# Kernel tuning notes

Hardware: AMD Instinct MI355X
Metric: run time of the kernel (lower is better)

Reference implementation:

```python
import jax, jax.numpy as jnp
import numpy as np

N, E, C, L, B = 40000, 640000, 128, 3, 64
EPS = 1e-5


def _layer_norm(h, g, b):
    m = h.mean(-1, keepdims=True)
    v = h.var(-1, keepdims=True)
    return (h - m) / jnp.sqrt(v + EPS) * g + b


def setup_inputs() -> dict:
    key = jax.random.key(0)
    ks = jax.random.split(key, 24)
    s = 0.05
    inp = {
        "x": jax.random.normal(ks[0], (N, C), jnp.float32),
        "edge_index": jax.random.randint(ks[1], (2, E), 0, N, dtype=jnp.int32),
        "batch": jnp.sort(jax.random.randint(ks[2], (N,), 0, B, dtype=jnp.int32)),
        # pre-scaler Linear(in=C -> hidden=C)
        "pre_w": jax.random.normal(ks[3], (C, C), jnp.float32) * s,
        "pre_b": jnp.zeros((C,), jnp.float32),
        # per-layer GCNConv weight/bias
        "conv_w": jax.random.normal(ks[4], (L, C, C), jnp.float32) * s,
        "conv_b": jnp.zeros((L, C), jnp.float32),
        # per-layer post-conv LayerNorm (applied for layers 0..L-2)
        "ln_g": jnp.ones((L, C), jnp.float32),
        "ln_b": jnp.zeros((L, C), jnp.float32),
        # per-layer FFN: lin1, lin2, LayerNorm
        "ffn_w1": jax.random.normal(ks[5], (L, C, C), jnp.float32) * s,
        "ffn_b1": jnp.zeros((L, C), jnp.float32),
        "ffn_w2": jax.random.normal(ks[6], (L, C, C), jnp.float32) * s,
        "ffn_b2": jnp.zeros((L, C), jnp.float32),
        "ffn_ln_g": jnp.ones((L, C), jnp.float32),
        "ffn_ln_b": jnp.zeros((L, C), jnp.float32),
        # classifier MLP: Linear(C,C)+ReLU+Linear(C,1)
        "cls_w1": jax.random.normal(ks[7], (C, C), jnp.float32) * s,
        "cls_b1": jnp.zeros((C,), jnp.float32),
        "cls_w2": jax.random.normal(ks[8], (C, 1), jnp.float32) * s,
        "cls_b2": jnp.zeros((1,), jnp.float32),
    }
    return inp


def reference(x, edge_index, batch, pre_w, pre_b, conv_w, conv_b, ln_g, ln_b,
              ffn_w1, ffn_b1, ffn_w2, ffn_b2, ffn_ln_g, ffn_ln_b,
              cls_w1, cls_b1, cls_w2, cls_b2):
    src, dst = edge_index[0], edge_index[1]
    # GCN symmetric normalization with self-loops: deg counts incoming edges + 1
    deg = jax.ops.segment_sum(jnp.ones((E,), x.dtype), dst, num_segments=N) + 1.0
    inv_sqrt = jax.lax.rsqrt(deg)                      # [N]
    norm_e = inv_sqrt[src] * inv_sqrt[dst]             # [E]
    self_norm = inv_sqrt * inv_sqrt                    # [N], 1/deg for self-loop

    h = x @ pre_w + pre_b                              # pre_scaler

    for i in range(L):
        layer_in = h
        hw = h @ conv_w[i]                             # [N,C]
        msg = hw[src] * norm_e[:, None]                # gather + scale [E,C]
        h = jax.ops.segment_sum(msg, dst, num_segments=N)
        h = h + hw * self_norm[:, None] + conv_b[i]    # self-loop + bias
        if i < L - 1:
            h = _layer_norm(h, ln_g[i], ln_b[i])       # norm
            h = jax.nn.relu(h)                         # act (act_first=False)
            h = h + layer_in                           # residual (dropout=0)
            # FFN: lin2(relu(lin1(h))) + h, then norm
            y = jax.nn.relu(h @ ffn_w1[i] + ffn_b1[i]) @ ffn_w2[i] + ffn_b2[i] + h
            h = _layer_norm(y, ffn_ln_g[i], ffn_ln_b[i])

    # global mean pool per graph
    counts = jax.ops.segment_sum(jnp.ones((N,), h.dtype), batch, num_segments=B)
    g = jax.ops.segment_sum(h, batch, num_segments=B) / jnp.maximum(counts, 1.0)[:, None]

    out = jax.nn.relu(g @ cls_w1 + cls_b1) @ cls_w2 + cls_b2   # [B,1]
    return out
```

## Files before the change

kernel.cpp:

```cpp
#include <hip/hip_runtime.h>
#include <hip/hip_fp16.h>
#include <cstdint>
#include <cstddef>

#define N_NODES 40000
#define N_EDGES 640000
#define CH 128
#define NL 3
#define NB 64
#define LN_EPS 1e-5f

typedef short short8 __attribute__((ext_vector_type(8)));
typedef float floatx4 __attribute__((ext_vector_type(4)));

__device__ __forceinline__ unsigned short bf16_rne(float f) {
    unsigned int u = __float_as_uint(f);
    unsigned int r = u + 0x7FFF + ((u >> 16) & 1);
    return (unsigned short)(r >> 16);
}


__global__ void deg_kernel(const int* __restrict__ ei, int* __restrict__ degi) {
    int e = blockIdx.x * 256 + threadIdx.x;
    if (e < N_EDGES) atomicAdd(&degi[ei[N_EDGES + e]], 1);
}

__global__ void isq_kernel(const int* __restrict__ degi, float* __restrict__ isq) {
    int n = blockIdx.x * 256 + threadIdx.x;
    if (n < N_NODES) isq[n] = rsqrtf((float)degi[n] + 1.0f);
}

__global__ void scan1_kernel(const int* __restrict__ degi, int* __restrict__ rowptr,
                             int* __restrict__ bsum) {
    __shared__ int s[256];
    int t = threadIdx.x;
    int i = blockIdx.x * 256 + t;
    int v = (i < N_NODES) ? degi[i] : 0;
    s[t] = v;
    __syncthreads();
    for (int off = 1; off < 256; off <<= 1) {
        int add = (t >= off) ? s[t - off] : 0;
        __syncthreads();
        s[t] += add;
        __syncthreads();
    }
    if (i < N_NODES) rowptr[i + 1] = s[t];
    if (t == 255) bsum[blockIdx.x] = s[255];
}

__global__ void scan2_kernel(int* __restrict__ bsum, int* __restrict__ boff, int nb) {
    __shared__ int s[256];
    int t = threadIdx.x;
    int v = (t < nb) ? bsum[t] : 0;
    s[t] = v;
    __syncthreads();
    for (int off = 1; off < 256; off <<= 1) {
        int add = (t >= off) ? s[t - off] : 0;
        __syncthreads();
        s[t] += add;
        __syncthreads();
    }
    if (t < nb) boff[t] = s[t] - v;
}

__global__ void scan3_kernel(int* __restrict__ rowptr, const int* __restrict__ boff) {
    int i = blockIdx.x * 256 + threadIdx.x;
    if (i < N_NODES) rowptr[i + 1] += boff[blockIdx.x];
    if (i == 0 && blockIdx.x == 0) rowptr[0] = 0;
}

__global__ void fill_csr_kernel(const int* __restrict__ ei, const int* __restrict__ rowptr,
                                int* __restrict__ fill, int* __restrict__ srcs) {
    int e = blockIdx.x * 256 + threadIdx.x;
    if (e < N_EDGES) {
        int s = ei[e];
        int d = ei[N_EDGES + e];
        int pos = atomicAdd(&fill[d], 1);
        srcs[rowptr[d] + pos] = s;
    }
}

__global__ void pack_w_kernel(const float* __restrict__ pre_w, const float* __restrict__ conv_w,
                              const float* __restrict__ ffn_w1, const float* __restrict__ ffn_w2,
                              short* __restrict__ wpk, float* __restrict__ zbias) {
    int idx = blockIdx.x * 256 + threadIdx.x;
    if (idx < CH) zbias[idx] = 0.f;
    int mat = idx >> 14;
    int e = idx & 16383;
    int k = e >> 7, n = e & 127;
    const float* src;
    switch (mat) {
        case 0: src = pre_w; break;
        case 1: case 2: case 3: src = conv_w + (size_t)(mat - 1) * 16384; break;
        case 4: case 5: src = ffn_w1 + (size_t)(mat - 4) * 16384; break;
        default: src = ffn_w2 + (size_t)(mat - 6) * 16384; break;
    }
    float f = src[e];
    unsigned short h = bf16_rne(f);
    float hf = __uint_as_float((unsigned)h << 16);
    unsigned short l = bf16_rne(f - hf);
    int kk = k >> 5, quad = (k >> 3) & 3, j = k & 7;
    int frag = ((kk * 4 + quad) * 128 + n) * 8 + j;
    wpk[(size_t)mat * 32768 + frag] = (short)h;
    wpk[(size_t)mat * 32768 + 16384 + frag] = (short)l;
}

__device__ __forceinline__ void gld_lds16(const short* g, short* l) {
    __builtin_amdgcn_global_load_lds(
        (const __attribute__((address_space(1))) unsigned int*)g,
        (__attribute__((address_space(3))) unsigned int*)l, 16, 0, 0);
}

template <int MODE, int OUTHALF>
__launch_bounds__(256, 3)
__global__ void gemm_mfma(const float* __restrict__ A, const short* __restrict__ Wpk,
                          const float* __restrict__ bias, const float* __restrict__ Res,
                          void* __restrict__ OutP) {
    __shared__ short smem[16384];
    const int tid = threadIdx.x;
    const int lane = tid & 63;
    const int wv = tid >> 6;
    const int row0 = blockIdx.x * 64 + wv * 16;
    const int m = lane & 15;
    const int quad = lane >> 4;

    floatx4 acc[8];
#pragma unroll
    for (int c = 0; c < 8; ++c) acc[c] = (floatx4){0.f, 0.f, 0.f, 0.f};

    const float* arow = A + (size_t)(row0 + m) * CH + quad * 8;

#pragma unroll 1
    for (int h = 0; h < 2; ++h) {
#pragma unroll
        for (int r = 0; r < 4; ++r) {
            int off = r * 2048 + tid * 8;
            gld_lds16(Wpk + h * 8192 + off, smem + off);
        }
#pragma unroll
        for (int r = 0; r < 4; ++r) {
            int off = r * 2048 + tid * 8;
            gld_lds16(Wpk + 16384 + h * 8192 + off, smem + 8192 + off);
        }
        __syncthreads();

#pragma unroll 1
        for (int kx = 0; kx < 2; ++kx) {
            const int kk = h * 2 + kx;
            float4 a0 = *(const float4*)(arow + kk * 32);
            float4 a1 = *(const float4*)(arow + kk * 32 + 4);
            float av[8] = {a0.x, a0.y, a0.z, a0.w, a1.x, a1.y, a1.z, a1.w};
            short8 ahi, alo;
#pragma unroll
            for (int j = 0; j < 8; ++j) {
                unsigned short hb = bf16_rne(av[j]);
                ahi[j] = (short)hb;
                alo[j] = (short)bf16_rne(av[j] - __uint_as_float((unsigned)hb << 16));
            }
            const short* sm_h = smem + ((kx * 4 + quad) * 128 + m) * 8;
            const short* sm_l = sm_h + 8192;
#pragma unroll
            for (int c = 0; c < 8; ++c) {
                short8 bhi = *(const short8*)(sm_h + c * 128);
                short8 blo = *(const short8*)(sm_l + c * 128);
                acc[c] = __builtin_amdgcn_mfma_f32_16x16x32_bf16(ahi, bhi, acc[c], 0, 0, 0);
                acc[c] = __builtin_amdgcn_mfma_f32_16x16x32_bf16(alo, bhi, acc[c], 0, 0, 0);
                acc[c] = __builtin_amdgcn_mfma_f32_16x16x32_bf16(ahi, blo, acc[c], 0, 0, 0);
            }
        }
        __syncthreads();
    }

#pragma unroll
    for (int c = 0; c < 8; ++c) {
        int col = c * 16 + m;
        float bv = bias[col];
#pragma unroll
        for (int r = 0; r < 4; ++r) {
            int row = row0 + quad * 4 + r;
            float v = acc[c][r] + bv;
            if (MODE == 1) v = fmaxf(v, 0.f);
            if (MODE == 2) v += Res[(size_t)row * CH + col];
            if (OUTHALF)
                ((__half*)OutP)[(size_t)row * CH + col] = __float2half(v);
            else
                ((float*)OutP)[(size_t)row * CH + col] = v;
        }
    }
}

template <int FUSED>
__launch_bounds__(256)
__global__ void agg_kernel(const __half* __restrict__ HW, const int* __restrict__ rowptr,
                           const int* __restrict__ srcs, const float* __restrict__ isq,
                           const float* __restrict__ bias, const float* __restrict__ gamma,
                           const float* __restrict__ beta, float* __restrict__ Hres,
                           float* __restrict__ Out) {
    const int lane = threadIdx.x & 63;
    const int node = blockIdx.x * 4 + (threadIdx.x >> 6);
    const int start = rowptr[node];
    const int end = rowptr[node + 1];

    float ax = 0.f, ay = 0.f;
    for (int base = start; base < end; base += 64) {
        int idx = base + lane;
        int clamped = (idx < end) ? idx : (end - 1);
        int sl = srcs[clamped];
        float wl = isq[sl];
        int cnt = end - base;
        if (cnt > 64) cnt = 64;
        int j = 0;
        for (; j + 4 <= cnt; j += 4) {
            int s0 = __shfl(sl, j), s1 = __shfl(sl, j + 1);
            int s2 = __shfl(sl, j + 2), s3 = __shfl(sl, j + 3);
            float w0 = __shfl(wl, j), w1 = __shfl(wl, j + 1);
            float w2 = __shfl(wl, j + 2), w3 = __shfl(wl, j + 3);
            float2 v0 = __half22float2(*(const __half2*)(HW + (size_t)s0 * CH + lane * 2));
            float2 v1 = __half22float2(*(const __half2*)(HW + (size_t)s1 * CH + lane * 2));
            float2 v2 = __half22float2(*(const __half2*)(HW + (size_t)s2 * CH + lane * 2));
            float2 v3 = __half22float2(*(const __half2*)(HW + (size_t)s3 * CH + lane * 2));
            ax = fmaf(w0, v0.x, ax); ay = fmaf(w0, v0.y, ay);
            ax = fmaf(w1, v1.x, ax); ay = fmaf(w1, v1.y, ay);
            ax = fmaf(w2, v2.x, ax); ay = fmaf(w2, v2.y, ay);
            ax = fmaf(w3, v3.x, ax); ay = fmaf(w3, v3.y, ay);
        }
        for (; j < cnt; ++j) {
            int s = __shfl(sl, j);
            float w = __shfl(wl, j);
            float2 vf = __half22float2(*(const __half2*)(HW + (size_t)s * CH + lane * 2));
            ax = fmaf(w, vf.x, ax);
            ay = fmaf(w, vf.y, ay);
        }
    }
    float d = isq[node];
    const __half2 hv = *(const __half2*)(HW + (size_t)node * CH + lane * 2);
    float2 hf = __half22float2(hv);
    const float2 bb = *(const float2*)(bias + lane * 2);
    float hx = d * ax + d * d * hf.x + bb.x;
    float hy = d * ay + d * d * hf.y + bb.y;

    if (!FUSED) {
        float2 o; o.x = hx; o.y = hy;
        *(float2*)(Out + (size_t)node * CH + lane * 2) = o;
        return;
    }
    float sum = hx + hy;
    float sq = hx * hx + hy * hy;
    for (int msk = 1; msk < 64; msk <<= 1) {
        sum += __shfl_xor(sum, msk);
        sq += __shfl_xor(sq, msk);
    }
    float mean = sum * (1.f / CH);
    float var = sq * (1.f / CH) - mean * mean;
    float rstd = rsqrtf(var + LN_EPS);
    const float2 gg = *(const float2*)(gamma + lane * 2);
    const float2 be = *(const float2*)(beta + lane * 2);
    float y0 = (hx - mean) * rstd * gg.x + be.x;
    float y1 = (hy - mean) * rstd * gg.y + be.y;
    float2* hp = (float2*)(Hres + (size_t)node * CH + lane * 2);
    float2 rr = *hp;
    float2 o;
    o.x = fmaxf(y0, 0.f) + rr.x;
    o.y = fmaxf(y1, 0.f) + rr.y;
    *hp = o;
}

__launch_bounds__(256)
__global__ void ln_kernel(float* __restrict__ D, const float* __restrict__ S,
                          const float* __restrict__ gamma, const float* __restrict__ beta) {
    const int lane = threadIdx.x & 63;
    const int node = blockIdx.x * 4 + (threadIdx.x >> 6);
    const float2 x = *(const float2*)(S + (size_t)node * CH + lane * 2);
    float sum = x.x + x.y;
    float sq = x.x * x.x + x.y * x.y;
    for (int msk = 1; msk < 64; msk <<= 1) {
        sum += __shfl_xor(sum, msk);
        sq += __shfl_xor(sq, msk);
    }
    float mean = sum * (1.f / CH);
    float var = sq * (1.f / CH) - mean * mean;
    float rstd = rsqrtf(var + LN_EPS);
    const float2 gg = *(const float2*)(gamma + lane * 2);
    const float2 bb = *(const float2*)(beta + lane * 2);
    float2 o;
    o.x = (x.x - mean) * rstd * gg.x + bb.x;
    o.y = (x.y - mean) * rstd * gg.y + bb.y;
    *(float2*)(D + (size_t)node * CH + lane * 2) = o;
}

__launch_bounds__(256)
__global__ void pool_kernel(const float* __restrict__ H, const int* __restrict__ batch,
                            float* __restrict__ g, float* __restrict__ cntf) {
    const int lane = threadIdx.x & 63;
    const int w = blockIdx.x * 4 + (threadIdx.x >> 6);
    const int n0 = w * 16;
    float lx = 0.f, ly = 0.f;
    int run = 0;
    int cur = batch[n0];
    for (int t = 0; t < 16; ++t) {
        int n = n0 + t;
        int b = batch[n];
        if (b != cur) {
            atomicAdd(&g[(size_t)cur * CH + lane * 2], lx);
            atomicAdd(&g[(size_t)cur * CH + lane * 2 + 1], ly);
            if (lane == 0) atomicAdd(&cntf[cur], (float)run);
            lx = ly = 0.f; run = 0; cur = b;
        }
        const float2 v = *(const float2*)(H + (size_t)n * CH + lane * 2);
        lx += v.x; ly += v.y; ++run;
    }
    atomicAdd(&g[(size_t)cur * CH + lane * 2], lx);
    atomicAdd(&g[(size_t)cur * CH + lane * 2 + 1], ly);
    if (lane == 0) atomicAdd(&cntf[cur], (float)run);
}

__launch_bounds__(128)
__global__ void cls_kernel(const float* __restrict__ g, const float* __restrict__ cntf,
                           const float* __restrict__ w1, const float* __restrict__ b1,
                           const float* __restrict__ w2, const float* __restrict__ b2,
                           float* __restrict__ out) {
    __shared__ float gm[CH];
    __shared__ float red[2];
    const int b = blockIdx.x;
    const int t = threadIdx.x;
    float inv = 1.f / fmaxf(cntf[b], 1.f);
    gm[t] = g[(size_t)b * CH + t] * inv;
    __syncthreads();
    float acc = b1[t];
    for (int k = 0; k < CH; ++k) acc = fmaf(gm[k], w1[(size_t)k * CH + t], acc);
    float v = fmaxf(acc, 0.f) * w2[t];
    for (int msk = 1; msk < 64; msk <<= 1) v += __shfl_xor(v, msk);
    if ((t & 63) == 0) red[t >> 6] = v;
    __syncthreads();
    if (t == 0) out[b] = red[0] + red[1] + b2[0];
}


extern "C" void kernel_launch(void* const* d_in, const int* in_sizes, int n_in,
                              void* d_out, int out_size, void* d_ws, size_t ws_size,
                              hipStream_t stream) {
    const float* x      = (const float*)d_in[0];
    const int*   ei     = (const int*)d_in[1];
    const int*   batch  = (const int*)d_in[2];
    const float* pre_w  = (const float*)d_in[3];
    const float* pre_b  = (const float*)d_in[4];
    const float* conv_w = (const float*)d_in[5];
    const float* conv_b = (const float*)d_in[6];
    const float* ln_g   = (const float*)d_in[7];
    const float* ln_b   = (const float*)d_in[8];
    const float* ffn_w1 = (const float*)d_in[9];
    const float* ffn_b1 = (const float*)d_in[10];
    const float* ffn_w2 = (const float*)d_in[11];
    const float* ffn_b2 = (const float*)d_in[12];
    const float* fln_g  = (const float*)d_in[13];
    const float* fln_b  = (const float*)d_in[14];
    const float* cls_w1 = (const float*)d_in[15];
    const float* cls_b1 = (const float*)d_in[16];
    const float* cls_w2 = (const float*)d_in[17];
    const float* cls_b2 = (const float*)d_in[18];

    float* H    = (float*)d_ws;
    float* T    = H + (size_t)N_NODES * CH;
    float* R    = T + (size_t)N_NODES * CH;
    __half* HWh = (__half*)R;
    int*   degi = (int*)(R + (size_t)N_NODES * CH);
    int*   fill = degi + N_NODES;
    float* g    = (float*)(fill + N_NODES);
    float* cntf = g + (size_t)NB * CH;
    float* isq  = cntf + NB;
    int*  rowptr = (int*)(isq + N_NODES);
    int*  bsum   = rowptr + N_NODES + 1;
    int*  boff   = bsum + 256;
    int*  srcs   = boff + 256;
    short* wpk   = (short*)(srcs + N_EDGES);
    float* zbias = (float*)(wpk + 8 * 32768);

    const int nb_scan = (N_NODES + 255) / 256;

    hipMemsetAsync(degi, 0, (size_t)(2 * N_NODES + NB * CH + NB) * sizeof(int), stream);

    deg_kernel<<<N_EDGES / 256, 256, 0, stream>>>(ei, degi);
    isq_kernel<<<nb_scan, 256, 0, stream>>>(degi, isq);
    scan1_kernel<<<nb_scan, 256, 0, stream>>>(degi, rowptr, bsum);
    scan2_kernel<<<1, 256, 0, stream>>>(bsum, boff, nb_scan);
    scan3_kernel<<<nb_scan, 256, 0, stream>>>(rowptr, boff);
    fill_csr_kernel<<<N_EDGES / 256, 256, 0, stream>>>(ei, rowptr, fill, srcs);
    pack_w_kernel<<<8 * 16384 / 256, 256, 0, stream>>>(pre_w, conv_w, ffn_w1, ffn_w2,
                                                       wpk, zbias);

    const int gblk = N_NODES / 64;
    const int lblk = N_NODES / 4;

    gemm_mfma<0, 0><<<gblk, 256, 0, stream>>>(x, wpk, pre_b, nullptr, H);

    for (int i = 0; i < NL; ++i) {
        gemm_mfma<0, 1><<<gblk, 256, 0, stream>>>(H, wpk + (size_t)(1 + i) * 32768,
                                                  zbias, nullptr, HWh);
        if (i < NL - 1) {
            agg_kernel<1><<<lblk, 256, 0, stream>>>(HWh, rowptr, srcs, isq,
                                                    conv_b + (size_t)i * CH,
                                                    ln_g + (size_t)i * CH,
                                                    ln_b + (size_t)i * CH, H, nullptr);
            gemm_mfma<1, 0><<<gblk, 256, 0, stream>>>(H, wpk + (size_t)(4 + i) * 32768,
                                                      ffn_b1 + (size_t)i * CH, nullptr, T);
            gemm_mfma<2, 0><<<gblk, 256, 0, stream>>>(T, wpk + (size_t)(6 + i) * 32768,
                                                      ffn_b2 + (size_t)i * CH, H, R);
            ln_kernel<<<lblk, 256, 0, stream>>>(H, R, fln_g + (size_t)i * CH,
                                                fln_b + (size_t)i * CH);
        } else {
            agg_kernel<0><<<lblk, 256, 0, stream>>>(HWh, rowptr, srcs, isq,
                                                    conv_b + (size_t)i * CH,
                                                    nullptr, nullptr, nullptr, T);
        }
    }

    pool_kernel<<<N_NODES / 64, 256, 0, stream>>>(T, batch, g, cntf);
    cls_kernel<<<NB, CH, 0, stream>>>(g, cntf, cls_w1, cls_b1, cls_w2, cls_b2,
                                      (float*)d_out);
}
```

Measured before the change: 392.6 us.

## Fuse back-to-back GEMMs with LayerNorm epilogue and fold isq into scan

Adds a kernel that runs two chained 128x128 GEMMs per 64-row tile, keeping the intermediate in LDS. It is used for the pre-scaler plus first conv projection, and for the FFN lin1/lin2 with residual and LayerNorm computed in the epilogue. This removes the global round trips of the FFN intermediate and the separate LN kernel. The isq kernel is merged into scan1. The costs are larger LDS use (about 66 KB per block) and lower occupancy, and the fused kernel reads and writes H in place, which is safe only because each block touches only its own rows.

```diff
diff --git a/kernel.cpp b/kernel.cpp
--- a/kernel.cpp
+++ b/kernel.cpp
@@ -9,6 +9,7 @@
 #define NL 3
 #define NB 64
 #define LN_EPS 1e-5f
+#define TSTRIDE 132
 
 typedef short short8 __attribute__((ext_vector_type(8)));
 typedef float floatx4 __attribute__((ext_vector_type(4)));
@@ -25,17 +26,13 @@
     if (e < N_EDGES) atomicAdd(&degi[ei[N_EDGES + e]], 1);
 }
 
-__global__ void isq_kernel(const int* __restrict__ degi, float* __restrict__ isq) {
-    int n = blockIdx.x * 256 + threadIdx.x;
-    if (n < N_NODES) isq[n] = rsqrtf((float)degi[n] + 1.0f);
-}
-
 __global__ void scan1_kernel(const int* __restrict__ degi, int* __restrict__ rowptr,
-                             int* __restrict__ bsum) {
+                             int* __restrict__ bsum, float* __restrict__ isq) {
     __shared__ int s[256];
     int t = threadIdx.x;
     int i = blockIdx.x * 256 + t;
     int v = (i < N_NODES) ? degi[i] : 0;
+    if (i < N_NODES) isq[i] = rsqrtf((float)v + 1.0f);
     s[t] = v;
     __syncthreads();
     for (int off = 1; off < 256; off <<= 1) {
@@ -105,6 +102,7 @@
     wpk[(size_t)mat * 32768 + 16384 + frag] = (short)l;
 }
 
+
 __device__ __forceinline__ void gld_lds16(const short* g, short* l) {
     __builtin_amdgcn_global_load_lds(
         (const __attribute__((address_space(1))) unsigned int*)g,
@@ -185,6 +183,174 @@
                 ((__half*)OutP)[(size_t)row * CH + col] = __float2half(v);
             else
                 ((float*)OutP)[(size_t)row * CH + col] = v;
+        }
+    }
+}
+
+template <int VARIANT>
+__launch_bounds__(256, 2)
+__global__ void gemm2_fused(const float* __restrict__ A, const short* __restrict__ W1pk,
+                            const float* __restrict__ b1, const short* __restrict__ W2pk,
+                            const float* __restrict__ b2, const float* __restrict__ Res,
+                            const float* __restrict__ gamma, const float* __restrict__ beta,
+                            float* __restrict__ OutG, void* __restrict__ OutP) {
+    __shared__ short wsm[16384];
+    __shared__ float tbuf[64 * TSTRIDE];
+    const int tid = threadIdx.x;
+    const int lane = tid & 63;
+    const int wv = tid >> 6;
+    const int row0 = blockIdx.x * 64 + wv * 16;
+    const int m = lane & 15;
+    const int quad = lane >> 4;
+
+    floatx4 acc[8];
+#pragma unroll
+    for (int c = 0; c < 8; ++c) acc[c] = (floatx4){0.f, 0.f, 0.f, 0.f};
+
+    const float* arow = A + (size_t)(row0 + m) * CH + quad * 8;
+
+#pragma unroll 1
+    for (int h = 0; h < 2; ++h) {
+#pragma unroll
+        for (int r = 0; r < 4; ++r) {
+            int off = r * 2048 + tid * 8;
+            gld_lds16(W1pk + h * 8192 + off, wsm + off);
+        }
+#pragma unroll
+        for (int r = 0; r < 4; ++r) {
+            int off = r * 2048 + tid * 8;
+            gld_lds16(W1pk + 16384 + h * 8192 + off, wsm + 8192 + off);
+        }
+        __syncthreads();
+
+#pragma unroll 1
+        for (int kx = 0; kx < 2; ++kx) {
+            const int kk = h * 2 + kx;
+            float4 a0 = *(const float4*)(arow + kk * 32);
+            float4 a1 = *(const float4*)(arow + kk * 32 + 4);
+            float av[8] = {a0.x, a0.y, a0.z, a0.w, a1.x, a1.y, a1.z, a1.w};
+            short8 ahi, alo;
+#pragma unroll
+            for (int j = 0; j < 8; ++j) {
+                unsigned short hb = bf16_rne(av[j]);
+                ahi[j] = (short)hb;
+                alo[j] = (short)bf16_rne(av[j] - __uint_as_float((unsigned)hb << 16));
+            }
+            const short* sm_h = wsm + ((kx * 4 + quad) * 128 + m) * 8;
+            const short* sm_l = sm_h + 8192;
+#pragma unroll
+            for (int c = 0; c < 8; ++c) {
+                short8 bhi = *(const short8*)(sm_h + c * 128);
+                short8 blo = *(const short8*)(sm_l + c * 128);
+                acc[c] = __builtin_amdgcn_mfma_f32_16x16x32_bf16(ahi, bhi, acc[c], 0, 0, 0);
+                acc[c] = __builtin_amdgcn_mfma_f32_16x16x32_bf16(alo, bhi, acc[c], 0, 0, 0);
+                acc[c] = __builtin_amdgcn_mfma_f32_16x16x32_bf16(ahi, blo, acc[c], 0, 0, 0);
+            }
+        }
+        __syncthreads();
+    }
+
+#pragma unroll
+    for (int c = 0; c < 8; ++c) {
+        int col = c * 16 + m;
+        float bv = b1[col];
+#pragma unroll
+        for (int r = 0; r < 4; ++r) {
+            int lrow = wv * 16 + quad * 4 + r;
+            float v = acc[c][r] + bv;
+            if (VARIANT == 1) v = fmaxf(v, 0.f);
+            tbuf[lrow * TSTRIDE + col] = v;
+            if (VARIANT == 0)
+                OutG[(size_t)(row0 + quad * 4 + r) * CH + col] = v;
+        }
+        acc[c] = (floatx4){0.f, 0.f, 0.f, 0.f};
+    }
+
+    const float* trow = tbuf + (wv * 16 + m) * TSTRIDE + quad * 8;
+#pragma unroll 1
+    for (int h = 0; h < 2; ++h) {
+#pragma unroll
+        for (int r = 0; r < 4; ++r) {
+            int off = r * 2048 + tid * 8;
+            gld_lds16(W2pk + h * 8192 + off, wsm + off);
+        }
+#pragma unroll
+        for (int r = 0; r < 4; ++r) {
+            int off = r * 2048 + tid * 8;
+            gld_lds16(W2pk + 16384 + h * 8192 + off, wsm + 8192 + off);
+        }
+        __syncthreads();
+
+#pragma unroll 1
+        for (int kx = 0; kx < 2; ++kx) {
+            const int kk = h * 2 + kx;
+            float av[8];
+#pragma unroll
+            for (int j = 0; j < 8; ++j) av[j] = trow[kk * 32 + j];
+            short8 ahi, alo;
+#pragma unroll
+            for (int j = 0; j < 8; ++j) {
+                unsigned short hb = bf16_rne(av[j]);
+                ahi[j] = (short)hb;
+                alo[j] = (short)bf16_rne(av[j] - __uint_as_float((unsigned)hb << 16));
+            }
+            const short* sm_h = wsm + ((kx * 4 + quad) * 128 + m) * 8;
+            const short* sm_l = sm_h + 8192;
+#pragma unroll
+            for (int c = 0; c < 8; ++c) {
+                short8 bhi = *(const short8*)(sm_h + c * 128);
+                short8 blo = *(const short8*)(sm_l + c * 128);
+                acc[c] = __builtin_amdgcn_mfma_f32_16x16x32_bf16(ahi, bhi, acc[c], 0, 0, 0);
+                acc[c] = __builtin_amdgcn_mfma_f32_16x16x32_bf16(alo, bhi, acc[c], 0, 0, 0);
+                acc[c] = __builtin_amdgcn_mfma_f32_16x16x32_bf16(ahi, blo, acc[c], 0, 0, 0);
+            }
+        }
+        __syncthreads();
+    }
+
+    if (VARIANT == 0) {
+#pragma unroll
+        for (int c = 0; c < 8; ++c) {
+            int col = c * 16 + m;
+#pragma unroll
+            for (int r = 0; r < 4; ++r) {
+                int row = row0 + quad * 4 + r;
+                ((__half*)OutP)[(size_t)row * CH + col] = __float2half(acc[c][r]);
+            }
+        }
+    } else {
+#pragma unroll
+        for (int c = 0; c < 8; ++c) {
+            int col = c * 16 + m;
+            float bv = b2[col];
+#pragma unroll
+            for (int r = 0; r < 4; ++r)
+                acc[c][r] += bv + Res[(size_t)(row0 + quad * 4 + r) * CH + col];
+        }
+#pragma unroll
+        for (int r = 0; r < 4; ++r) {
+            float s = 0.f, q = 0.f;
+#pragma unroll
+            for (int c = 0; c < 8; ++c) {
+                float t = acc[c][r];
+                s += t;
+                q = fmaf(t, t, q);
+            }
+#pragma unroll
+            for (int msk = 1; msk < 16; msk <<= 1) {
+                s += __shfl_xor(s, msk);
+                q += __shfl_xor(q, msk);
+            }
+            float mean = s * (1.f / CH);
+            float var = q * (1.f / CH) - mean * mean;
+            float rstd = rsqrtf(var + LN_EPS);
+            int row = row0 + quad * 4 + r;
+#pragma unroll
+            for (int c = 0; c < 8; ++c) {
+                int col = c * 16 + m;
+                float y = (acc[c][r] - mean) * rstd * gamma[col] + beta[col];
+                ((float*)OutP)[(size_t)row * CH + col] = y;
+            }
         }
     }
 }
@@ -266,29 +432,6 @@
 }
 
 __launch_bounds__(256)
-__global__ void ln_kernel(float* __restrict__ D, const float* __restrict__ S,
-                          const float* __restrict__ gamma, const float* __restrict__ beta) {
-    const int lane = threadIdx.x & 63;
-    const int node = blockIdx.x * 4 + (threadIdx.x >> 6);
-    const float2 x = *(const float2*)(S + (size_t)node * CH + lane * 2);
-    float sum = x.x + x.y;
-    float sq = x.x * x.x + x.y * x.y;
-    for (int msk = 1; msk < 64; msk <<= 1) {
-        sum += __shfl_xor(sum, msk);
-        sq += __shfl_xor(sq, msk);
-    }
-    float mean = sum * (1.f / CH);
-    float var = sq * (1.f / CH) - mean * mean;
-    float rstd = rsqrtf(var + LN_EPS);
-    const float2 gg = *(const float2*)(gamma + lane * 2);
-    const float2 bb = *(const float2*)(beta + lane * 2);
-    float2 o;
-    o.x = (x.x - mean) * rstd * gg.x + bb.x;
-    o.y = (x.y - mean) * rstd * gg.y + bb.y;
-    *(float2*)(D + (size_t)node * CH + lane * 2) = o;
-}
-
-__launch_bounds__(256)
 __global__ void pool_kernel(const float* __restrict__ H, const int* __restrict__ batch,
                             float* __restrict__ g, float* __restrict__ cntf) {
     const int lane = threadIdx.x & 63;
@@ -380,8 +523,7 @@
     hipMemsetAsync(degi, 0, (size_t)(2 * N_NODES + NB * CH + NB) * sizeof(int), stream);
 
     deg_kernel<<<N_EDGES / 256, 256, 0, stream>>>(ei, degi);
-    isq_kernel<<<nb_scan, 256, 0, stream>>>(degi, isq);
-    scan1_kernel<<<nb_scan, 256, 0, stream>>>(degi, rowptr, bsum);
+    scan1_kernel<<<nb_scan, 256, 0, stream>>>(degi, rowptr, bsum, isq);
     scan2_kernel<<<1, 256, 0, stream>>>(bsum, boff, nb_scan);
     scan3_kernel<<<nb_scan, 256, 0, stream>>>(rowptr, boff);
     fill_csr_kernel<<<N_EDGES / 256, 256, 0, stream>>>(ei, rowptr, fill, srcs);
@@ -391,22 +533,27 @@
     const int gblk = N_NODES / 64;
     const int lblk = N_NODES / 4;
 
-    gemm_mfma<0, 0><<<gblk, 256, 0, stream>>>(x, wpk, pre_b, nullptr, H);
+    gemm2_fused<0><<<gblk, 256, 0, stream>>>(x, wpk, pre_b,
+                                             wpk + 1 * 32768, nullptr, nullptr,
+                                             nullptr, nullptr, H, HWh);
 
     for (int i = 0; i < NL; ++i) {
-        gemm_mfma<0, 1><<<gblk, 256, 0, stream>>>(H, wpk + (size_t)(1 + i) * 32768,
-                                                  zbias, nullptr, HWh);
+        if (i > 0) {
+            gemm_mfma<0, 1><<<gblk, 256, 0, stream>>>(H, wpk + (size_t)(1 + i) * 32768,
+                                                      zbias, nullptr, HWh);
+        }
         if (i < NL - 1) {
             agg_kernel<1><<<lblk, 256, 0, stream>>>(HWh, rowptr, srcs, isq,
                                                     conv_b + (size_t)i * CH,
                                                     ln_g + (size_t)i * CH,
                                                     ln_b + (size_t)i * CH, H, nullptr);
-            gemm_mfma<1, 0><<<gblk, 256, 0, stream>>>(H, wpk + (size_t)(4 + i) * 32768,
-                                                      ffn_b1 + (size_t)i * CH, nullptr, T);
-            gemm_mfma<2, 0><<<gblk, 256, 0, stream>>>(T, wpk + (size_t)(6 + i) * 32768,
-                                                      ffn_b2 + (size_t)i * CH, H, R);
-            ln_kernel<<<lblk, 256, 0, stream>>>(H, R, fln_g + (size_t)i * CH,
-                                                fln_b + (size_t)i * CH);
+            gemm2_fused<1><<<gblk, 256, 0, stream>>>(H, wpk + (size_t)(4 + i) * 32768,
+                                                     ffn_b1 + (size_t)i * CH,
+                                                     wpk + (size_t)(6 + i) * 32768,
+                                                     ffn_b2 + (size_t)i * CH, H,
+                                                     fln_g + (size_t)i * CH,
+                                                     fln_b + (size_t)i * CH,
+                                                     nullptr, H);
         } else {
             agg_kernel<0><<<lblk, 256, 0, stream>>>(HWh, rowptr, srcs, isq,
                                                     conv_b + (size_t)i * CH,
```

Measured after the change: 367.0 us. -6.5%, faster.
